# Performance work log

Measured on AMD Instinct MI355X. Metric: run time of the kernel, lower is better.

## Reference

```python
import jax, jax.numpy as jnp
import numpy as np

B, N, E = 8, 4096, 131072
NODE_DIM, HIDDEN = 64, 128


def _mlp2(x, W1, b1, W2, b2):
    # Linear -> SiLU -> Linear
    return jax.nn.silu(x @ W1 + b1) @ W2 + b2


def setup_inputs() -> dict:
    key = jax.random.key(0)
    ks = jax.random.split(key, 10)
    inp = {
        "node_features": jax.random.normal(ks[0], (B, N, NODE_DIM), jnp.float32),
        "coords": jax.random.normal(ks[1], (B, N, 3), jnp.float32),
        "edge_index": jax.random.randint(ks[2], (2, E), 0, N, jnp.int32),
        # message_net: in = 2*node_dim + 1 = 129
        "Wm1": jax.random.normal(ks[3], (2 * NODE_DIM + 1, HIDDEN), jnp.float32) * 0.05,
        "bm1": jnp.zeros((HIDDEN,), jnp.float32),
        "Wm2": jax.random.normal(ks[4], (HIDDEN, HIDDEN), jnp.float32) * 0.05,
        "bm2": jnp.zeros((HIDDEN,), jnp.float32),
        # node_update: in = node_dim + hidden = 192
        "Wn1": jax.random.normal(ks[5], (NODE_DIM + HIDDEN, HIDDEN), jnp.float32) * 0.05,
        "bn1": jnp.zeros((HIDDEN,), jnp.float32),
        "Wn2": jax.random.normal(ks[6], (HIDDEN, NODE_DIM), jnp.float32) * 0.05,
        "bn2": jnp.zeros((NODE_DIM,), jnp.float32),
        # coord_update: hidden -> hidden -> 1
        "Wc1": jax.random.normal(ks[7], (HIDDEN, HIDDEN), jnp.float32) * 0.05,
        "bc1": jnp.zeros((HIDDEN,), jnp.float32),
        "Wc2": jax.random.normal(ks[8], (HIDDEN, 1), jnp.float32) * 0.05,
        "bc2": jnp.zeros((1,), jnp.float32),
    }
    return inp


def reference(node_features, coords, edge_index, Wm1, bm1, Wm2, bm2,
              Wn1, bn1, Wn2, bn2, Wc1, bc1, Wc2, bc2):
    src, dst = edge_index[0], edge_index[1]
    # Gather per-edge geometry: [B, E, 3]
    edge_vec = coords[:, dst, :] - coords[:, src, :]
    edge_dist = jnp.linalg.norm(edge_vec, axis=-1, keepdims=True)  # [B,E,1]
    edge_vec_n = edge_vec / (edge_dist + 1e-8)
    # Gather node features per edge and build message input: [B, E, 2*D+1]
    msg_in = jnp.concatenate(
        [node_features[:, src, :], node_features[:, dst, :], edge_dist], axis=-1)
    messages = _mlp2(msg_in, Wm1, bm1, Wm2, bm2)  # [B, E, H]
    # Scatter-add messages into destination nodes: [B, N, H]
    agg = jnp.zeros((node_features.shape[0], node_features.shape[1], messages.shape[-1]),
                    dtype=messages.dtype).at[:, dst, :].add(messages)
    # Residual node update
    nf_new = node_features + _mlp2(
        jnp.concatenate([node_features, agg], axis=-1), Wn1, bn1, Wn2, bn2)
    # Equivariant coordinate update
    coord_w = _mlp2(messages, Wc1, bc1, Wc2, bc2)  # [B, E, 1]
    coord_delta = jnp.zeros_like(coords).at[:, dst, :].add(coord_w * edge_vec_n)
    coords_new = coords + coord_delta
    return nf_new, coords_new
```

## Files before the change

kernel.cpp:

```cpp
#include <hip/hip_runtime.h>
#include <hip/hip_bf16.h>

#define B_ 8
#define N_ 4096
#define E_ 131072
#define D_ 64
#define H_ 128

#define EDGE_BLOCKS 256
#define ETILE 128
#define TILES_TOTAL ((B_ * E_) / ETILE)
#define TILES_PER_BLOCK (TILES_TOTAL / EDGE_BLOCKS)

typedef unsigned int u32;
typedef short bf16x8 __attribute__((ext_vector_type(8)));
typedef float f32x4 __attribute__((ext_vector_type(4)));

__device__ __forceinline__ unsigned short f2bf(float f) {
  u32 x = __float_as_uint(f);
  x += 0x7fffu + ((x >> 16) & 1u);
  return (unsigned short)(x >> 16);
}
__device__ __forceinline__ float bf2f(unsigned short v) {
  return __uint_as_float(((u32)v) << 16);
}
__device__ __forceinline__ u32 cvt_pk_bf16(float lo, float hi) {
  u32 r;
  asm("v_cvt_pk_bf16_f32 %0, %1, %2" : "=v"(r) : "v"(lo), "v"(hi));
  return r;
}
__device__ __forceinline__ float silu_f(float x) { return x / (1.0f + __expf(-x)); }

__device__ __forceinline__ int swz(int row, int col) {
  return row * 128 + (col ^ ((row & 7) << 3));
}

#define MFMA(a, b, c) __builtin_amdgcn_mfma_f32_16x16x32_bf16(a, b, c, 0, 0, 0)

__global__ __launch_bounds__(512) void p12_k(
    const float* __restrict__ nf, const float* __restrict__ Wm1,
    const float* __restrict__ bm1,
    unsigned short* __restrict__ P1, unsigned short* __restrict__ P2)
{
  __shared__ unsigned short sWa[128 * 64];
  __shared__ unsigned short sWb[128 * 64];
  __shared__ unsigned short sNf[64 * 64];

  const int tid = threadIdx.x;
  const int node0 = blockIdx.x * 64;

  for (int i = tid; i < 64 * 128; i += 512) {
    const int k = i >> 7, n = i & 127;
    const int d = n * 64 + (k ^ ((n & 7) << 3));
    sWa[d] = f2bf(Wm1[k * 128 + n]);
    sWb[d] = f2bf(Wm1[(64 + k) * 128 + n]);
  }
  {
    const int row = tid >> 3, c0 = 8 * (tid & 7);
    const float4 v0 = *(const float4*)&nf[(size_t)(node0 + row) * 64 + c0];
    const float4 v1 = *(const float4*)&nf[(size_t)(node0 + row) * 64 + c0 + 4];
    uint4 pk = make_uint4(cvt_pk_bf16(v0.x, v0.y), cvt_pk_bf16(v0.z, v0.w),
                          cvt_pk_bf16(v1.x, v1.y), cvt_pk_bf16(v1.z, v1.w));
    *(uint4*)&sNf[row * 64 + (c0 ^ ((row & 7) << 3))] = pk;
  }
  __syncthreads();

  const int lane = tid & 63;
  const int w = tid >> 6;
  const int l15 = lane & 15;
  const int l4 = lane >> 4;
  const int k0l = l4 * 8;
  const int colbase = (w & 3) * 32;
  const int n0 = colbase + l15, n1 = n0 + 16;
  const unsigned short* sW = (w < 4) ? sWa : sWb;
  const float add0 = (w < 4) ? bm1[n0] : 0.f;
  const float add1 = (w < 4) ? bm1[n1] : 0.f;
  unsigned short* OUT = (w < 4) ? P1 : P2;

  f32x4 acc[4][2];
  {
    f32x4 z = {0.f, 0.f, 0.f, 0.f};
#pragma unroll
    for (int i = 0; i < 4; ++i) { acc[i][0] = z; acc[i][1] = z; }
  }
#pragma unroll
  for (int ks = 0; ks < 2; ++ks) {
    const int k = ks * 32 + k0l;
    bf16x8 b0 = *(const bf16x8*)&sW[n0 * 64 + (k ^ ((n0 & 7) << 3))];
    bf16x8 b1 = *(const bf16x8*)&sW[n1 * 64 + (k ^ ((n1 & 7) << 3))];
#pragma unroll
    for (int i = 0; i < 4; ++i) {
      const int row = 16 * i + l15;
      bf16x8 a = *(const bf16x8*)&sNf[row * 64 + (k ^ ((row & 7) << 3))];
      acc[i][0] = MFMA(a, b0, acc[i][0]);
      acc[i][1] = MFMA(a, b1, acc[i][1]);
    }
  }
#pragma unroll
  for (int i = 0; i < 4; ++i)
#pragma unroll
    for (int r = 0; r < 4; ++r) {
      const int m = 16 * i + l4 * 4 + r;
      OUT[(size_t)(node0 + m) * 128 + n0] = f2bf(acc[i][0][r] + add0);
      OUT[(size_t)(node0 + m) * 128 + n1] = f2bf(acc[i][1][r] + add1);
    }
}

__global__ void hist_k(const int* __restrict__ ei, int* __restrict__ hist) {
  const int e = blockIdx.x * 256 + threadIdx.x;
  atomicAdd(&hist[ei[E_ + e]], 1);
}

__global__ __launch_bounds__(1024) void scan4096(int* __restrict__ h) {
  __shared__ int wsums[16];
  const int tid = threadIdx.x;
  const int lane = tid & 63, wv = tid >> 6;
  int4 v = ((int4*)h)[tid];
  const int s = v.x + v.y + v.z + v.w;
  int incl = s;
#pragma unroll
  for (int off = 1; off < 64; off <<= 1) {
    int u = __shfl_up(incl, off);
    if (lane >= off) incl += u;
  }
  if (lane == 63) wsums[wv] = incl;
  __syncthreads();
  if (wv == 0) {
    int ws = (lane < 16) ? wsums[lane] : 0;
#pragma unroll
    for (int off = 1; off < 16; off <<= 1) {
      int u = __shfl_up(ws, off);
      if (lane >= off) ws += u;
    }
    if (lane < 16) wsums[lane] = ws;
  }
  __syncthreads();
  int base = (wv ? wsums[wv - 1] : 0) + (incl - s);
  int4 o;
  o.x = base; o.y = base + v.x; o.z = o.y + v.y; o.w = o.z + v.z;
  ((int4*)h)[tid] = o;
}

__global__ void scatter_k(const int* __restrict__ ei, int* __restrict__ offs,
                          int* __restrict__ src_s, int* __restrict__ dst_s) {
  const int e = blockIdx.x * 256 + threadIdx.x;
  const int d = ei[E_ + e];
  const int p = atomicAdd(&offs[d], 1);
  src_s[p] = ei[e];
  dst_s[p] = d;
}

__global__ __launch_bounds__(1024, 4) void egnn_edge_mfma(
    const unsigned short* __restrict__ P1, const unsigned short* __restrict__ P2,
    const float* __restrict__ coords,
    const int* __restrict__ src_s, const int* __restrict__ dst_s,
    const float* __restrict__ Wm1,
    const float* __restrict__ Wm2, const float* __restrict__ bm2,
    const float* __restrict__ Wc1, const float* __restrict__ bc1,
    const float* __restrict__ Wc2, const float* __restrict__ bc2,
    float* __restrict__ agg, float* __restrict__ cdelta)
{
  __shared__ unsigned short sW2[128 * 128];
  __shared__ unsigned short sW3[128 * 128];
  __shared__ unsigned short bufA[ETILE * 128];
  __shared__ unsigned short bufB[ETILE * 128];
  __shared__ float swr[128];
  __shared__ float4 sgeo[2][ETILE];
  __shared__ int sdst[2][ETILE];
  __shared__ float swpart[4][ETILE];

  const int tid = threadIdx.x;
  for (int i = tid; i < 128 * 128; i += 1024) {
    const int k = i >> 7, n = i & 127;
    const int d = swz(n, k);
    sW2[d] = f2bf(Wm2[i]);
    sW3[d] = f2bf(Wc1[i]);
  }
  if (tid < 128) swr[tid] = Wm1[128 * 128 + tid];

  const int lane = tid & 63;
  const int w = tid >> 6;
  const int l15 = lane & 15;
  const int l4 = lane >> 4;
  const int k0l = l4 * 8;
  const int rowbase = (w >> 2) * 32;
  const int colbase = (w & 3) * 32;
  const int rA = rowbase + l15;
  const int rB = colbase + l15;
  const int n0 = colbase + l15;
  const int n1 = n0 + 16;

  const float bb2_0 = bm2[n0], bb2_1 = bm2[n1];
  const float bb3_0 = bc1[n0], bb3_1 = bc1[n1];
  const float wc2_0 = Wc2[n0], wc2_1 = Wc2[n1];
  const float bc2v = bc2[0];

  const int m_t = tid >> 3;
  const int q_t = tid & 7;

  const int myblk = (blockIdx.x & 7) * (EDGE_BLOCKS / 8) + (blockIdx.x >> 3);
  const int b = myblk >> 5;
  const int gbase = (myblk & 31) * TILES_PER_BLOCK;

  __syncthreads();

  f32x4 acc[2][2];

  for (int t = 0; t < TILES_PER_BLOCK; ++t) {
    const int p = t & 1;
    const int ebase = (gbase + t) * ETILE;

    {
      const int e = ebase + m_t;
      const int s = src_s[e];
      const int d = dst_s[e];
      const float* cs = coords + (size_t)(b * N_ + s) * 3;
      const float* cd = coords + (size_t)(b * N_ + d) * 3;
      const float d0 = cd[0] - cs[0], d1 = cd[1] - cs[1], d2 = cd[2] - cs[2];
      const float dist = sqrtf(fmaf(d0, d0, fmaf(d1, d1, d2 * d2)));
      if (q_t == 0) {
        sdst[p][m_t] = d;
        sgeo[p][m_t] = make_float4(d0, d1, d2, dist);
      }
      const int c0 = 16 * q_t;
      const uint4* p1p = (const uint4*)(P1 + (size_t)(b * N_ + s) * 128 + c0);
      const uint4* p2p = (const uint4*)(P2 + (size_t)(b * N_ + d) * 128 + c0);
      uint4 xa = p1p[0], xb = p1p[1];
      uint4 ya = p2p[0], yb = p2p[1];
      u32 opk[8];
#pragma unroll
      for (int jj = 0; jj < 4; ++jj) {
        const float2 wr2 = *(const float2*)&swr[c0 + 2 * jj];
        const u32 xp = ((const u32*)&xa)[jj], yp = ((const u32*)&ya)[jj];
        const float lo = bf2f((unsigned short)xp) + bf2f((unsigned short)yp) + dist * wr2.x;
        const float hi = bf2f((unsigned short)(xp >> 16)) + bf2f((unsigned short)(yp >> 16)) + dist * wr2.y;
        opk[jj] = cvt_pk_bf16(silu_f(lo), silu_f(hi));
      }
#pragma unroll
      for (int jj = 0; jj < 4; ++jj) {
        const float2 wr2 = *(const float2*)&swr[c0 + 8 + 2 * jj];
        const u32 xp = ((const u32*)&xb)[jj], yp = ((const u32*)&yb)[jj];
        const float lo = bf2f((unsigned short)xp) + bf2f((unsigned short)yp) + dist * wr2.x;
        const float hi = bf2f((unsigned short)(xp >> 16)) + bf2f((unsigned short)(yp >> 16)) + dist * wr2.y;
        opk[4 + jj] = cvt_pk_bf16(silu_f(lo), silu_f(hi));
      }
      *(uint4*)&bufA[swz(m_t, c0)] = make_uint4(opk[0], opk[1], opk[2], opk[3]);
      *(uint4*)&bufA[swz(m_t, c0 + 8)] = make_uint4(opk[4], opk[5], opk[6], opk[7]);
    }
    __syncthreads();

    {
      f32x4 z = {0.f, 0.f, 0.f, 0.f};
      acc[0][0] = z; acc[0][1] = z; acc[1][0] = z; acc[1][1] = z;
    }
#pragma unroll
    for (int ks = 0; ks < 4; ++ks) {
      const int k = ks * 32 + k0l;
      bf16x8 b0 = *(const bf16x8*)&sW2[swz(rB, k)];
      bf16x8 b1 = *(const bf16x8*)&sW2[swz(rB + 16, k)];
      bf16x8 a0 = *(const bf16x8*)&bufA[swz(rA, k)];
      bf16x8 a1 = *(const bf16x8*)&bufA[swz(rA + 16, k)];
      acc[0][0] = MFMA(a0, b0, acc[0][0]);
      acc[0][1] = MFMA(a0, b1, acc[0][1]);
      acc[1][0] = MFMA(a1, b0, acc[1][0]);
      acc[1][1] = MFMA(a1, b1, acc[1][1]);
    }
#pragma unroll
    for (int i = 0; i < 2; ++i)
#pragma unroll
      for (int r = 0; r < 4; ++r) {
        const int m = rowbase + 16 * i + l4 * 4 + r;
        const u32 pk = cvt_pk_bf16(acc[i][0][r] + bb2_0, acc[i][1][r] + bb2_1);
        bufB[swz(m, n0)] = (unsigned short)pk;
        bufB[swz(m, n1)] = (unsigned short)(pk >> 16);
      }
    __syncthreads();

    {
      f32x4 z = {0.f, 0.f, 0.f, 0.f};
      acc[0][0] = z; acc[0][1] = z; acc[1][0] = z; acc[1][1] = z;
    }
#pragma unroll
    for (int ks = 0; ks < 4; ++ks) {
      const int k = ks * 32 + k0l;
      bf16x8 b0 = *(const bf16x8*)&sW3[swz(rB, k)];
      bf16x8 b1 = *(const bf16x8*)&sW3[swz(rB + 16, k)];
      bf16x8 a0 = *(const bf16x8*)&bufB[swz(rA, k)];
      bf16x8 a1 = *(const bf16x8*)&bufB[swz(rA + 16, k)];
      acc[0][0] = MFMA(a0, b0, acc[0][0]);
      acc[0][1] = MFMA(a0, b1, acc[0][1]);
      acc[1][0] = MFMA(a1, b0, acc[1][0]);
      acc[1][1] = MFMA(a1, b1, acc[1][1]);
    }
#pragma unroll
    for (int i = 0; i < 2; ++i)
#pragma unroll
      for (int r = 0; r < 4; ++r) {
        float pw = silu_f(acc[i][0][r] + bb3_0) * wc2_0 +
                   silu_f(acc[i][1][r] + bb3_1) * wc2_1;
        pw += __shfl_xor(pw, 1);
        pw += __shfl_xor(pw, 2);
        pw += __shfl_xor(pw, 4);
        pw += __shfl_xor(pw, 8);
        if (l15 == 0) swpart[w & 3][rowbase + 16 * i + l4 * 4 + r] = pw;
      }

    {
      const int c0 = 2 * (tid & 63);
      int r = (tid >> 6) * 8;
      int cur = sdst[p][r];
      float a0s = 0.f, a1s = 0.f;
#pragma unroll 4
      for (int k = 0; k < 8; ++k, ++r) {
        const int d2 = sdst[p][r];
        if (d2 != cur) {
          float* bp2 = agg + ((size_t)(b * N_ + cur)) * H_ + c0;
          unsafeAtomicAdd(bp2, a0s);
          unsafeAtomicAdd(bp2 + 1, a1s);
          a0s = 0.f; a1s = 0.f;
          cur = d2;
        }
        const u32 pkr = *(const u32*)&bufB[swz(r, c0)];
        a0s += bf2f((unsigned short)pkr);
        a1s += bf2f((unsigned short)(pkr >> 16));
      }
      float* bp2 = agg + ((size_t)(b * N_ + cur)) * H_ + c0;
      unsafeAtomicAdd(bp2, a0s);
      unsafeAtomicAdd(bp2 + 1, a1s);
    }
    __syncthreads();

    if (tid < ETILE) {
      float wc = bc2v;
#pragma unroll
      for (int cg = 0; cg < 4; ++cg) wc += swpart[cg][tid];
      const float4 g = sgeo[p][tid];
      const float inv = 1.0f / (g.w + 1e-8f);
      float vx = wc * g.x * inv, vy = wc * g.y * inv, vz = wc * g.z * inv;
      const int myd = sdst[p][tid];
      int flg = (lane == 0) ? 1 : (sdst[p][tid - 1] != myd);
#pragma unroll
      for (int off = 1; off < 64; off <<= 1) {
        float ux = __shfl_up(vx, off);
        float uy = __shfl_up(vy, off);
        float uz = __shfl_up(vz, off);
        int uf = __shfl_up(flg, off);
        if (lane >= off) {
          if (!flg) { vx += ux; vy += uy; vz += uz; }
          flg |= uf;
        }
      }
      const bool tail = (lane == 63) || (sdst[p][tid + 1] != myd);
      if (tail) {
        float* bp = cdelta + ((size_t)(b * N_ + myd)) * 3;
        unsafeAtomicAdd(bp + 0, vx);
        unsafeAtomicAdd(bp + 1, vy);
        unsafeAtomicAdd(bp + 2, vz);
      }
    }
  }
}

#define NTILE 128

__global__ __launch_bounds__(512) void egnn_node_mfma(
    const float* __restrict__ nf, const float* __restrict__ coords,
    const float* __restrict__ agg, const float* __restrict__ cdelta,
    const float* __restrict__ Wn1, const float* __restrict__ bn1,
    const float* __restrict__ Wn2, const float* __restrict__ bn2,
    float* __restrict__ out_nf, float* __restrict__ out_c)
{
  __shared__ unsigned short sA[128 * 192];
  __shared__ unsigned short sB[64 * 128];
  __shared__ unsigned short bufN[128 * 64];
  __shared__ unsigned short bufA[128 * 128];
  __shared__ unsigned short hbuf[128 * 128];

  const int tid = threadIdx.x;
  const int node0 = blockIdx.x * NTILE;

  for (int i = tid; i < 192 * 128; i += 512) {
    const int k = i >> 7, n = i & 127;
    sA[n * 192 + (k ^ ((n & 7) << 3))] = f2bf(Wn1[i]);
  }
  for (int i = tid; i < 128 * 64; i += 512) {
    const int k = i >> 6, n = i & 63;
    sB[n * 128 + (k ^ ((n & 7) << 3))] = f2bf(Wn2[i]);
  }
#pragma unroll
  for (int j = 0; j < 8; ++j) {
    const int p = tid + j * 512;
    const int row = p >> 5, col = 2 * (p & 31);
    float2 v = *(const float2*)&nf[(size_t)(node0 + row) * 64 + col];
    *(u32*)&bufN[row * 64 + (col ^ ((row & 7) << 3))] = cvt_pk_bf16(v.x, v.y);
  }
#pragma unroll
  for (int j = 0; j < 16; ++j) {
    const int p = tid + j * 512;
    const int row = p >> 6, col = 2 * (p & 63);
    float2 v = *(const float2*)&agg[(size_t)(node0 + row) * 128 + col];
    *(u32*)&bufA[row * 128 + (col ^ ((row & 7) << 3))] = cvt_pk_bf16(v.x, v.y);
  }
  if (tid < 3 * NTILE) {
    out_c[(size_t)node0 * 3 + tid] =
        coords[(size_t)node0 * 3 + tid] + cdelta[(size_t)node0 * 3 + tid];
  }

  const int lane = tid & 63;
  const int w = tid >> 6;
  const int l15 = lane & 15;
  const int l4 = lane >> 4;
  const int k0l = l4 * 8;

  const int rb1 = (w & 1) * 64;
  const int cb1 = (w >> 1) * 32;
  const int n0 = cb1 + l15, n1 = n0 + 16;
  const float bb1_0 = bn1[n0], bb1_1 = bn1[n1];

  const int rb2 = (w >> 1) * 32;
  const int cb2 = (w & 1) * 32;
  const int n20 = cb2 + l15, n21 = n20 + 16;
  const float bb2_0 = bn2[n20], bb2_1 = bn2[n21];

  __syncthreads();

  f32x4 acc[4][2];
  {
    f32x4 z = {0.f, 0.f, 0.f, 0.f};
#pragma unroll
    for (int i = 0; i < 4; ++i) { acc[i][0] = z; acc[i][1] = z; }
  }
#pragma unroll
  for (int ks = 0; ks < 2; ++ks) {
    const int k = ks * 32 + k0l;
    bf16x8 b0 = *(const bf16x8*)&sA[n0 * 192 + (k ^ ((n0 & 7) << 3))];
    bf16x8 b1 = *(const bf16x8*)&sA[n1 * 192 + (k ^ ((n1 & 7) << 3))];
#pragma unroll
    for (int i = 0; i < 4; ++i) {
      const int row = rb1 + 16 * i + l15;
      bf16x8 a = *(const bf16x8*)&bufN[row * 64 + (k ^ ((row & 7) << 3))];
      acc[i][0] = MFMA(a, b0, acc[i][0]);
      acc[i][1] = MFMA(a, b1, acc[i][1]);
    }
  }
#pragma unroll
  for (int ks = 0; ks < 4; ++ks) {
    const int k = ks * 32 + k0l;
    const int kg = 64 + k;
    bf16x8 b0 = *(const bf16x8*)&sA[n0 * 192 + (kg ^ ((n0 & 7) << 3))];
    bf16x8 b1 = *(const bf16x8*)&sA[n1 * 192 + (kg ^ ((n1 & 7) << 3))];
#pragma unroll
    for (int i = 0; i < 4; ++i) {
      const int row = rb1 + 16 * i + l15;
      bf16x8 a = *(const bf16x8*)&bufA[row * 128 + (k ^ ((row & 7) << 3))];
      acc[i][0] = MFMA(a, b0, acc[i][0]);
      acc[i][1] = MFMA(a, b1, acc[i][1]);
    }
  }
#pragma unroll
  for (int i = 0; i < 4; ++i)
#pragma unroll
    for (int r = 0; r < 4; ++r) {
      const int m = rb1 + 16 * i + l4 * 4 + r;
      hbuf[m * 128 + (n0 ^ ((m & 7) << 3))] = f2bf(silu_f(acc[i][0][r] + bb1_0));
      hbuf[m * 128 + (n1 ^ ((m & 7) << 3))] = f2bf(silu_f(acc[i][1][r] + bb1_1));
    }
  __syncthreads();

  {
    f32x4 z = {0.f, 0.f, 0.f, 0.f};
    acc[0][0] = z; acc[0][1] = z; acc[1][0] = z; acc[1][1] = z;
  }
#pragma unroll
  for (int ks = 0; ks < 4; ++ks) {
    const int k = ks * 32 + k0l;
    bf16x8 b0 = *(const bf16x8*)&sB[n20 * 128 + (k ^ ((n20 & 7) << 3))];
    bf16x8 b1 = *(const bf16x8*)&sB[n21 * 128 + (k ^ ((n21 & 7) << 3))];
    const int r0 = rb2 + l15, r1 = rb2 + 16 + l15;
    bf16x8 a0 = *(const bf16x8*)&hbuf[r0 * 128 + (k ^ ((r0 & 7) << 3))];
    bf16x8 a1 = *(const bf16x8*)&hbuf[r1 * 128 + (k ^ ((r1 & 7) << 3))];
    acc[0][0] = MFMA(a0, b0, acc[0][0]);
    acc[0][1] = MFMA(a0, b1, acc[0][1]);
    acc[1][0] = MFMA(a1, b0, acc[1][0]);
    acc[1][1] = MFMA(a1, b1, acc[1][1]);
  }
#pragma unroll
  for (int i = 0; i < 2; ++i)
#pragma unroll
    for (int r = 0; r < 4; ++r) {
      const int m = rb2 + 16 * i + l4 * 4 + r;
      const size_t base = (size_t)(node0 + m) * 64;
      out_nf[base + n20] = nf[base + n20] + acc[i][0][r] + bb2_0;
      out_nf[base + n21] = nf[base + n21] + acc[i][1][r] + bb2_1;
    }
}

extern "C" void kernel_launch(void* const* d_in, const int* in_sizes, int n_in,
                              void* d_out, int out_size, void* d_ws, size_t ws_size,
                              hipStream_t stream) {
  const float* nf     = (const float*)d_in[0];
  const float* coords = (const float*)d_in[1];
  const int*   ei     = (const int*)d_in[2];
  const float* Wm1 = (const float*)d_in[3];
  const float* bm1 = (const float*)d_in[4];
  const float* Wm2 = (const float*)d_in[5];
  const float* bm2 = (const float*)d_in[6];
  const float* Wn1 = (const float*)d_in[7];
  const float* bn1 = (const float*)d_in[8];
  const float* Wn2 = (const float*)d_in[9];
  const float* bn2 = (const float*)d_in[10];
  const float* Wc1 = (const float*)d_in[11];
  const float* bc1 = (const float*)d_in[12];
  const float* Wc2 = (const float*)d_in[13];
  const float* bc2 = (const float*)d_in[14];

  float* agg    = (float*)d_ws;
  float* cdelta = agg + (size_t)B_ * N_ * H_;
  int*   hist   = (int*)(cdelta + (size_t)B_ * N_ * 3);
  int*   src_s  = hist + 4096;
  int*   dst_s  = src_s + E_;
  unsigned short* P2 = (unsigned short*)(dst_s + E_);

  float* out_nf = (float*)d_out;
  float* out_c  = out_nf + (size_t)B_ * N_ * D_;

  unsigned short* P1 = (unsigned short*)d_out;

  const size_t zero_bytes =
      ((size_t)B_ * N_ * H_ + (size_t)B_ * N_ * 3 + 4096) * sizeof(float);
  hipMemsetAsync(d_ws, 0, zero_bytes, stream);

  p12_k<<<(B_ * N_) / 64, 512, 0, stream>>>(nf, Wm1, bm1, P1, P2);
  hist_k<<<E_ / 256, 256, 0, stream>>>(ei, hist);
  scan4096<<<1, 1024, 0, stream>>>(hist);
  scatter_k<<<E_ / 256, 256, 0, stream>>>(ei, hist, src_s, dst_s);

  egnn_edge_mfma<<<EDGE_BLOCKS, 1024, 0, stream>>>(
      P1, P2, coords, src_s, dst_s, Wm1, Wm2, bm2, Wc1, bc1, Wc2, bc2,
      agg, cdelta);
  egnn_node_mfma<<<(B_ * N_) / NTILE, 512, 0, stream>>>(
      nf, coords, agg, cdelta, Wn1, bn1, Wn2, bn2, out_nf, out_c);
}
```

Baseline: 371.9 us.

## Halve edge tile, use 512-thread blocks, keep Wc1 fragments in registers

New measurement: 398.8 us. 1.07x slower.

```diff
diff --git a/kernel.cpp b/kernel.cpp
--- a/kernel.cpp
+++ b/kernel.cpp
@@ -7,8 +7,8 @@
 #define D_ 64
 #define H_ 128
 
-#define EDGE_BLOCKS 256
-#define ETILE 128
+#define EDGE_BLOCKS 1024
+#define ETILE 64
 #define TILES_TOTAL ((B_ * E_) / ETILE)
 #define TILES_PER_BLOCK (TILES_TOTAL / EDGE_BLOCKS)
 
@@ -150,7 +150,7 @@
   dst_s[p] = d;
 }
 
-__global__ __launch_bounds__(1024, 4) void egnn_edge_mfma(
+__global__ __launch_bounds__(512, 4) void egnn_edge_mfma(
     const unsigned short* __restrict__ P1, const unsigned short* __restrict__ P2,
     const float* __restrict__ coords,
     const int* __restrict__ src_s, const int* __restrict__ dst_s,
@@ -161,20 +161,17 @@
     float* __restrict__ agg, float* __restrict__ cdelta)
 {
   __shared__ unsigned short sW2[128 * 128];
-  __shared__ unsigned short sW3[128 * 128];
   __shared__ unsigned short bufA[ETILE * 128];
   __shared__ unsigned short bufB[ETILE * 128];
   __shared__ float swr[128];
   __shared__ float4 sgeo[2][ETILE];
   __shared__ int sdst[2][ETILE];
-  __shared__ float swpart[4][ETILE];
+  __shared__ float swpart[8][ETILE];
 
   const int tid = threadIdx.x;
-  for (int i = tid; i < 128 * 128; i += 1024) {
+  for (int i = tid; i < 128 * 128; i += 512) {
     const int k = i >> 7, n = i & 127;
-    const int d = swz(n, k);
-    sW2[d] = f2bf(Wm2[i]);
-    sW3[d] = f2bf(Wc1[i]);
+    sW2[swz(n, k)] = f2bf(Wm2[i]);
   }
   if (tid < 128) swr[tid] = Wm1[128 * 128 + tid];
 
@@ -189,18 +186,29 @@
   const int rB = colbase + l15;
   const int n0 = colbase + l15;
   const int n1 = n0 + 16;
+  const int n3 = w * 16 + l15;
 
   const float bb2_0 = bm2[n0], bb2_1 = bm2[n1];
-  const float bb3_0 = bc1[n0], bb3_1 = bc1[n1];
-  const float wc2_0 = Wc2[n0], wc2_1 = Wc2[n1];
+  const float bb3 = bc1[n3];
+  const float wc2v = Wc2[n3];
   const float bc2v = bc2[0];
+
+  bf16x8 w3f[4];
+#pragma unroll
+  for (int ks = 0; ks < 4; ++ks) {
+    bf16x8 v;
+#pragma unroll
+    for (int j = 0; j < 8; ++j)
+      v[j] = (short)f2bf(Wc1[(ks * 32 + k0l + j) * 128 + n3]);
+    w3f[ks] = v;
+  }
 
   const int m_t = tid >> 3;
   const int q_t = tid & 7;
 
   const int myblk = (blockIdx.x & 7) * (EDGE_BLOCKS / 8) + (blockIdx.x >> 3);
-  const int b = myblk >> 5;
-  const int gbase = (myblk & 31) * TILES_PER_BLOCK;
+  const int b = myblk >> 7;
+  const int gbase = (myblk & 127) * TILES_PER_BLOCK;
 
   __syncthreads();
 
@@ -277,33 +285,32 @@
     __syncthreads();
 
     {
-      f32x4 z = {0.f, 0.f, 0.f, 0.f};
-      acc[0][0] = z; acc[0][1] = z; acc[1][0] = z; acc[1][1] = z;
-    }
-#pragma unroll
-    for (int ks = 0; ks < 4; ++ks) {
-      const int k = ks * 32 + k0l;
-      bf16x8 b0 = *(const bf16x8*)&sW3[swz(rB, k)];
-      bf16x8 b1 = *(const bf16x8*)&sW3[swz(rB + 16, k)];
-      bf16x8 a0 = *(const bf16x8*)&bufB[swz(rA, k)];
-      bf16x8 a1 = *(const bf16x8*)&bufB[swz(rA + 16, k)];
-      acc[0][0] = MFMA(a0, b0, acc[0][0]);
-      acc[0][1] = MFMA(a0, b1, acc[0][1]);
-      acc[1][0] = MFMA(a1, b0, acc[1][0]);
-      acc[1][1] = MFMA(a1, b1, acc[1][1]);
-    }
-#pragma unroll
-    for (int i = 0; i < 2; ++i)
-#pragma unroll
-      for (int r = 0; r < 4; ++r) {
-        float pw = silu_f(acc[i][0][r] + bb3_0) * wc2_0 +
-                   silu_f(acc[i][1][r] + bb3_1) * wc2_1;
-        pw += __shfl_xor(pw, 1);
-        pw += __shfl_xor(pw, 2);
-        pw += __shfl_xor(pw, 4);
-        pw += __shfl_xor(pw, 8);
-        if (l15 == 0) swpart[w & 3][rowbase + 16 * i + l4 * 4 + r] = pw;
-      }
+      f32x4 acc3[4];
+      {
+        f32x4 z = {0.f, 0.f, 0.f, 0.f};
+        acc3[0] = z; acc3[1] = z; acc3[2] = z; acc3[3] = z;
+      }
+#pragma unroll
+      for (int ks = 0; ks < 4; ++ks) {
+        const int k = ks * 32 + k0l;
+#pragma unroll
+        for (int i = 0; i < 4; ++i) {
+          bf16x8 a = *(const bf16x8*)&bufB[swz(16 * i + l15, k)];
+          acc3[i] = MFMA(a, w3f[ks], acc3[i]);
+        }
+      }
+#pragma unroll
+      for (int i = 0; i < 4; ++i)
+#pragma unroll
+        for (int r = 0; r < 4; ++r) {
+          float pw = silu_f(acc3[i][r] + bb3) * wc2v;
+          pw += __shfl_xor(pw, 1);
+          pw += __shfl_xor(pw, 2);
+          pw += __shfl_xor(pw, 4);
+          pw += __shfl_xor(pw, 8);
+          if (l15 == 0) swpart[w][16 * i + l4 * 4 + r] = pw;
+        }
+    }
 
     {
       const int c0 = 2 * (tid & 63);
@@ -333,12 +340,12 @@
     if (tid < ETILE) {
       float wc = bc2v;
 #pragma unroll
-      for (int cg = 0; cg < 4; ++cg) wc += swpart[cg][tid];
+      for (int cg = 0; cg < 8; ++cg) wc += swpart[cg][tid];
       const float4 g = sgeo[p][tid];
       const float inv = 1.0f / (g.w + 1e-8f);
       float vx = wc * g.x * inv, vy = wc * g.y * inv, vz = wc * g.z * inv;
       const int myd = sdst[p][tid];
-      int flg = (lane == 0) ? 1 : (sdst[p][tid - 1] != myd);
+      int flg = (tid == 0) ? 1 : (sdst[p][tid - 1] != myd);
 #pragma unroll
       for (int off = 1; off < 64; off <<= 1) {
         float ux = __shfl_up(vx, off);
@@ -350,7 +357,7 @@
           flg |= uf;
         }
       }
-      const bool tail = (lane == 63) || (sdst[p][tid + 1] != myd);
+      const bool tail = (tid == ETILE - 1) || (sdst[p][tid + 1] != myd);
       if (tail) {
         float* bp = cdelta + ((size_t)(b * N_ + myd)) * 3;
         unsafeAtomicAdd(bp + 0, vx);
@@ -535,7 +542,7 @@
   scan4096<<<1, 1024, 0, stream>>>(hist);
   scatter_k<<<E_ / 256, 256, 0, stream>>>(ei, hist, src_s, dst_s);
 
-  egnn_edge_mfma<<<EDGE_BLOCKS, 1024, 0, stream>>>(
+  egnn_edge_mfma<<<EDGE_BLOCKS, 512, 0, stream>>>(
       P1, P2, coords, src_s, dst_s, Wm1, Wm2, bm2, Wc1, bc1, Wc2, bc2,
       agg, cdelta);
   egnn_node_mfma<<<(B_ * N_) / NTILE, 512, 0, stream>>>(
```
